# Kernel tuning notes

Hardware: AMD Instinct MI355X
Metric: run time of the kernel (lower is better)

Reference implementation:

```python
import jax, jax.numpy as jnp
import numpy as np

FEAT, HID, HEADS, OUT, NLAYERS = 32, 64, 6, 1, 4
NG, NP, K = 16, 1000, 10
EPS_BN, EPS_IN = 1e-5, 1e-5


def _build_graph(pos, rng=None):
    # knn_graph(k=10, loop=True, batch=batch) -> to_undirected -> add_self_loops
    N = NG * NP
    parts = []
    for g in range(NG):
        off = g * NP
        p = pos[off:off + NP]
        d2 = ((p[:, None, :] - p[None, :, :]) ** 2).sum(-1)
        nbr = np.argsort(d2, axis=1)[:, :K] + off  # includes self (loop=True)
        src = nbr.reshape(-1)
        dst = np.repeat(np.arange(NP) + off, K)
        parts.append(np.stack([src, dst]))
    ei = np.concatenate(parts, axis=1)
    und = np.unique(np.concatenate([ei, ei[::-1]], axis=1).T, axis=0).T  # to_undirected (coalesced)
    loops = np.tile(np.arange(N), (2, 1))  # add_self_loops (PyG appends unconditionally)
    return np.concatenate([und, loops], axis=1).astype(np.int64)


def setup_inputs() -> dict:
    rng = np.random.default_rng(0)
    N = NG * NP
    pos = rng.standard_normal((N, 3)).astype(np.float32)
    batch = np.repeat(np.arange(NG), NP).astype(np.int64)
    edge_index = _build_graph(pos)

    def lin(fi, fo):
        return (rng.standard_normal((fi, fo)) / np.sqrt(fi)).astype(np.float32)

    HC = HEADS * HID
    z = lambda *s: jnp.zeros(s, jnp.float32)
    o = lambda *s: jnp.ones(s, jnp.float32)
    return dict(
        x=jnp.asarray(rng.standard_normal((N, FEAT)).astype(np.float32)),
        pos=jnp.asarray(pos),
        w_lin1=jnp.asarray(lin(FEAT, HID)), b_lin1=z(HID),
        w_e1=jnp.asarray(lin(1, 32)), b_e1=z(32),
        w_e2=jnp.asarray(lin(32, 1)), b_e2=z(1),
        Wl=jnp.asarray(np.stack([lin(HID, HC) for _ in range(NLAYERS)])), bl=z(NLAYERS, HC),
        Wr=jnp.asarray(np.stack([lin(HID, HC) for _ in range(NLAYERS)])), br=z(NLAYERS, HC),
        We=jnp.asarray(np.stack([lin(1, HC) for _ in range(NLAYERS)])),
        att=jnp.asarray((rng.standard_normal((NLAYERS, HEADS, HID)) / np.sqrt(HID)).astype(np.float32)),
        b_gat=z(NLAYERS, HID),
        w_emb1=jnp.asarray(lin(HID, HID)), b_emb1=z(HID),
        bn1_g=o(HID), bn1_b=z(HID), bn1_m=z(HID), bn1_v=o(HID),
        w_emb2=jnp.asarray(lin(HID, HID)), b_emb2=z(HID),
        bn2_g=o(HID), bn2_b=z(HID), bn2_m=z(HID), bn2_v=o(HID),
        w_pred=jnp.asarray(lin(HID, OUT)), b_pred=z(OUT),
        edge_index=jnp.asarray(edge_index),
        batch=jnp.asarray(batch),
        n_graphs=NG,
    )


def _bn_eval(x, g, b, m, v):
    return (x - m) / jnp.sqrt(v + EPS_BN) * g + b


def _inorm(h, batch, n_graphs):
    # PyG InstanceNorm (affine=False): per-graph, per-channel standardization
    ones = jnp.ones((h.shape[0], 1), h.dtype)
    cnt = jax.ops.segment_sum(ones, batch, num_segments=n_graphs)
    mean = jax.ops.segment_sum(h, batch, num_segments=n_graphs) / cnt
    hc = h - mean[batch]
    var = jax.ops.segment_sum(hc * hc, batch, num_segments=n_graphs) / cnt
    return hc / jnp.sqrt(var[batch] + EPS_IN)


def _gatv2(h, src, dst, ea, Wl, bl, Wr, br, We, att, bias, n):
    # GATv2Conv(heads=HEADS, concat=False, edge_dim=1)
    xl = (h @ Wl + bl).reshape(-1, HEADS, HID)  # [N,H,C] source proj
    xr = (h @ Wr + br).reshape(-1, HEADS, HID)  # [N,H,C] target proj
    e = (ea @ We).reshape(-1, HEADS, HID)       # [E,H,C] edge proj (bias=False)
    g = jax.nn.leaky_relu(xl[src] + xr[dst] + e, 0.2)
    alpha = jnp.einsum('ehc,hc->eh', g, att)    # [E,H]
    amax = jax.ops.segment_max(alpha, dst, num_segments=n)
    ex = jnp.exp(alpha - amax[dst])
    den = jax.ops.segment_sum(ex, dst, num_segments=n)
    a = ex / (den[dst] + 1e-16)                 # PyG softmax eps
    out = jax.ops.segment_sum(xl[src] * a[:, :, None], dst, num_segments=n)
    return out.mean(axis=1) + bias              # concat=False -> head mean


def reference(x, pos, w_lin1, b_lin1, w_e1, b_e1, w_e2, b_e2, Wl, bl, Wr, br, We, att, b_gat,
              w_emb1, b_emb1, bn1_g, bn1_b, bn1_m, bn1_v, w_emb2, b_emb2,
              bn2_g, bn2_b, bn2_m, bn2_v, w_pred, b_pred, edge_index, batch, n_graphs):
    src, dst = edge_index[0], edge_index[1]
    d = pos[src] - pos[dst]
    s = (d * d).sum(-1, keepdims=True)
    ew = jnp.where(s == 0, 0.0, jnp.sqrt(jnp.where(s == 0, 1.0, s)))  # safe norm (0-grad at 0)
    m = jax.nn.relu(ew @ w_e1 + b_e1)            # MLP([1,32,1]) (BN in eval = identity)
    ea = jax.nn.relu(m @ w_e2 + b_e2)            # relu(edge_MLP(.)) -> [E,1]
    h = x @ w_lin1 + b_lin1
    n = h.shape[0]
    for i in range(NLAYERS):
        h = jax.nn.relu(h + _gatv2(h, src, dst, ea, Wl[i], bl[i], Wr[i], br[i], We[i], att[i], b_gat[i], n))
        h = _inorm(h, batch, n_graphs)
    z = jax.nn.relu(h @ w_emb1 + b_emb1)
    z = _bn_eval(z, bn1_g, bn1_b, bn1_m, bn1_v)
    h_out = z @ w_emb2 + b_emb2
    pred = _bn_eval(h_out, bn2_g, bn2_b, bn2_m, bn2_v) @ w_pred + b_pred
    return h_out, pred
```

## Files before the change

kernel.cpp:

```cpp
#include <hip/hip_runtime.h>
#include <hip/hip_bf16.h>
#include <stdint.h>

typedef __hip_bfloat16 bf16;
typedef __attribute__((ext_vector_type(8))) short short8;
typedef __attribute__((ext_vector_type(4))) float float4v;
__device__ __forceinline__ float bf(const bf16 x){ return __bfloat162float(x); }
__device__ __forceinline__ float bfu(uint32_t u){ u <<= 16; return __uint_as_float(u); }
__device__ __forceinline__ short f2bs(float v){
    bf16 b = __float2bfloat16(v);
    return *(short*)&b;
}

#define FEAT    32
#define HID     64
#define HEADS   6
#define HC      384
#define NLAYERS 4
#define NG      16
#define NP      1000
#define NN      16000
#define EPS_BN  1e-5f
#define EPS_IN  1e-5f
#define MNODE   16
#define LOG2E   1.44269504f
#define STATSZ  (2*NG*HID)
#define NBLK    (NN/4)

__device__ __forceinline__ float normv(float v, const float* st, int g, int c){
    if (!st) return v;
    float s  = st[g*HID + c];
    float s2 = st[NG*HID + g*HID + c];
    float mean = s*(1.f/NP);
    float var  = fmaxf(s2*(1.f/NP) - mean*mean, 0.f);
    return (v - mean)*rsqrtf(var + EPS_IN);
}

__global__ void sentinel_kernel(float* out, int n, float val){
    int i = blockIdx.x*256 + threadIdx.x;
    if (i < n) out[i] = val;
}

__global__ void zero_kernel(int* p, int n){
    int i = blockIdx.x*256 + threadIdx.x;
    if (i < n) p[i] = 0;
}

__global__ void detect_kernel(const int* ei, int* mode){
    __shared__ int nz;
    if (threadIdx.x == 0) nz = 0;
    __syncthreads();
    for (int i = 1 + 2*threadIdx.x; i < 1024; i += 512)
        if (ei[i] != 0) atomicAdd(&nz, 1);
    __syncthreads();
    if (threadIdx.x == 0) *mode = (nz == 0) ? 1 : 0;
}

__device__ __forceinline__ int load_idx(const int* ei, int idx, int mode){
    if (mode) return (int)((const long long*)ei)[idx];
    return ei[idx];
}

__global__ void count_kernel(const int* ei, const int* mode, int* deg, int E){
    int e = blockIdx.x*256 + threadIdx.x;
    if (e >= E) return;
    int d = load_idx(ei, E + e, *mode);
    if (d >= 0 && d < NN) atomicAdd(&deg[d], 1);
}

__global__ void scan_kernel(const int* deg, int* rowptr, int N){
    __shared__ int part[256];
    __shared__ int offs[256];
    int t = threadIdx.x;
    int chunk = (N + 255)/256;
    int lo = t*chunk, hi = lo + chunk; if (hi > N) hi = N;
    int s = 0;
    for (int i = lo; i < hi; i++) s += deg[i];
    part[t] = s;
    __syncthreads();
    if (t == 0){
        int r = 0;
        for (int i = 0; i < 256; i++){ offs[i] = r; r += part[i]; }
        rowptr[N] = r;
    }
    __syncthreads();
    int r = offs[t];
    for (int i = lo; i < hi; i++){ rowptr[i] = r; r += deg[i]; }
}

__global__ void scatter_ea_kernel(const int* ei, const float* pos,
                                  const float* w_e1, const float* b_e1,
                                  const float* w_e2, const float* b_e2,
                                  const int* rowptr, int* fill, const int* mode_p,
                                  int* csr_src, float* ea_csr, int E){
    int e = blockIdx.x*256 + threadIdx.x;
    if (e >= E) return;
    int mode = *mode_p;
    int s = load_idx(ei, e, mode);
    int d = load_idx(ei, E + e, mode);
    if (s < 0 || s >= NN || d < 0 || d >= NN) return;
    float dx = pos[s*3+0] - pos[d*3+0];
    float dy = pos[s*3+1] - pos[d*3+1];
    float dz = pos[s*3+2] - pos[d*3+2];
    float ss = dx*dx + dy*dy + dz*dz;
    float ew = (ss == 0.f) ? 0.f : sqrtf(ss);
    float acc = b_e2[0];
    #pragma unroll
    for (int j = 0; j < 32; j++){
        float m = ew*w_e1[j] + b_e1[j];
        m = m > 0.f ? m : 0.f;
        acc += m*w_e2[j];
    }
    acc = acc > 0.f ? acc : 0.f;
    int p = rowptr[d] + atomicAdd(&fill[d], 1);
    if (p < 0 || p >= E) return;
    csr_src[p] = s;
    ea_csr[p] = acc;
}

__global__ void lin1_kernel(const float* __restrict__ x,
                            const float* __restrict__ w1, const float* __restrict__ b1,
                            float* __restrict__ h, int N){
    int tid = blockIdx.x*256 + threadIdx.x;
    if (tid >= N*HID) return;
    int n = tid >> 6, c = tid & 63;
    float acc = b1[c];
    #pragma unroll
    for (int k = 0; k < FEAT; k++) acc += x[n*FEAT+k] * w1[k*HID+c];
    h[tid] = acc;
}

__global__ __launch_bounds__(256) void xlxr_mfma_kernel(
        const float* __restrict__ h, const float* __restrict__ statPrev,
        const float* __restrict__ Wl, const float* __restrict__ bl,
        const float* __restrict__ Wr, const float* __restrict__ br,
        bf16* __restrict__ xl, bf16* __restrict__ xr, int layer){
    int n0 = blockIdx.x*16;
    int wave = threadIdx.x >> 6;
    int lane = threadIdx.x & 63;
    int q = lane >> 4;
    int m = lane & 15;
    int node = n0 + m;
    int g = node / NP;

    short8 afrag[2];
    #pragma unroll
    for (int s = 0; s < 2; s++){
        const float* hp = h + (size_t)node*HID + s*32 + q*8;
        #pragma unroll
        for (int j = 0; j < 8; j++){
            float v = normv(hp[j], statPrev, g, s*32 + q*8 + j);
            afrag[s][j] = f2bs(v);
        }
    }

    const float* wlp = Wl + (size_t)layer*HID*HC;
    const float* wrp = Wr + (size_t)layer*HID*HC;
    const float* blp = bl + (size_t)layer*HC;
    const float* brp = br + (size_t)layer*HC;

    for (int t = wave*12; t < wave*12 + 12; t++){
        int col = t*16 + m;
        bool isR = col >= HC;
        int c2 = isR ? col - HC : col;
        const float* W = isR ? wrp : wlp;
        short8 bfrag[2];
        #pragma unroll
        for (int s = 0; s < 2; s++){
            #pragma unroll
            for (int j = 0; j < 8; j++)
                bfrag[s][j] = f2bs(W[(size_t)(s*32 + q*8 + j)*HC + c2]);
        }
        float4v acc = {0.f, 0.f, 0.f, 0.f};
        acc = __builtin_amdgcn_mfma_f32_16x16x32_bf16(afrag[0], bfrag[0], acc, 0, 0, 0);
        acc = __builtin_amdgcn_mfma_f32_16x16x32_bf16(afrag[1], bfrag[1], acc, 0, 0, 0);
        float bias = isR ? brp[c2] : blp[c2];
        bf16* dst = isR ? xr : xl;
        #pragma unroll
        for (int r = 0; r < 4; r++){
            int row = q*4 + r;
            dst[(size_t)(n0 + row)*HC + c2] = __float2bfloat16(acc[r] + bias);
        }
    }
}

__global__ __launch_bounds__(384) void xlxr_fb_kernel(
        const float* __restrict__ h, const float* __restrict__ statPrev,
        const float* __restrict__ Wl, const float* __restrict__ bl,
        bf16* __restrict__ xl, int layer){
    int n0 = blockIdx.x*MNODE;
    int o = threadIdx.x;
    __shared__ float hh[MNODE*HID];
    for (int i = o; i < MNODE*HID; i += 384){
        int m = i >> 6, k = i & 63;
        int node = n0 + m;
        hh[k*MNODE + m] = normv(h[(size_t)node*HID + k], statPrev, node/NP, k);
    }
    __syncthreads();
    const float* wl = Wl + (size_t)layer*HID*HC;
    float accl[MNODE];
    float bL = bl[layer*HC + o];
    #pragma unroll
    for (int m = 0; m < MNODE; m++) accl[m] = bL;
    for (int k = 0; k < HID; k++){
        float wlv = wl[k*HC + o];
        #pragma unroll
        for (int m = 0; m < MNODE; m++) accl[m] += hh[k*MNODE + m]*wlv;
    }
    #pragma unroll
    for (int m = 0; m < MNODE; m++)
        xl[(size_t)(n0+m)*HC + o] = __float2bfloat16(accl[m]);
}

__global__ __launch_bounds__(256) void agg_kernel(
        const bf16* __restrict__ xl, const bf16* __restrict__ xr,
        const int* __restrict__ rowptr,
        const int* __restrict__ csr_src,
        const float* __restrict__ ea_csr,
        const float* __restrict__ Wr, const float* __restrict__ br,
        const float* __restrict__ We, const float* __restrict__ att,
        const float* __restrict__ b_gat,
        float* __restrict__ h,
        const float* __restrict__ statPrev, float* __restrict__ partial,
        int layer){
    int wave = threadIdx.x >> 6, lane = threadIdx.x & 63;
    int n = blockIdx.x*4 + wave;
    int g = n / NP;
    int r0 = rowptr[n];
    int deg = rowptr[n+1] - r0;

    __shared__ float ps[4][2][HID];

    int hb = lane >> 5;
    int ob = hb*HID + ((lane & 31) << 1);

    float xrr[6], wer[6], atr[6];
    if (xr){
        const uint32_t* xr32 = (const uint32_t*)xr + (size_t)n*(HC/2);
        uint32_t u0 = xr32[lane], u1 = xr32[lane+64], u2 = xr32[lane+128];
        xrr[0] = bfu(u0 & 0xffffu); xrr[1] = bfu(u0 >> 16);
        xrr[2] = bfu(u1 & 0xffffu); xrr[3] = bfu(u1 >> 16);
        xrr[4] = bfu(u2 & 0xffffu); xrr[5] = bfu(u2 >> 16);
    } else {
        float hval = normv(h[(size_t)n*HID + lane], statPrev, g, lane);
        const float* wr = Wr + (size_t)layer*HID*HC;
        #pragma unroll
        for (int q = 0; q < 6; q++) xrr[q] = 0.f;
        for (int k = 0; k < HID; k++){
            float hk = __shfl(hval, k);
            #pragma unroll
            for (int q = 0; q < 3; q++){
                xrr[2*q]   += hk*wr[k*HC + ob + q*128];
                xrr[2*q+1] += hk*wr[k*HC + ob + q*128 + 1];
            }
        }
        #pragma unroll
        for (int q = 0; q < 3; q++){
            xrr[2*q]   += br[layer*HC + ob + q*128];
            xrr[2*q+1] += br[layer*HC + ob + q*128 + 1];
        }
    }
    #pragma unroll
    for (int q = 0; q < 3; q++){
        int o = layer*HC + ob + q*128;
        wer[2*q] = We[o];  wer[2*q+1] = We[o+1];
        atr[2*q] = att[o]*LOG2E; atr[2*q+1] = att[o+1]*LOG2E;
    }

    float m0 = -1e30f, m1 = -1e30f, m2 = -1e30f;
    float l0 = 0.f, l1 = 0.f, l2 = 0.f;
    float a0=0.f,a1=0.f,a2=0.f,a3=0.f,a4=0.f,a5=0.f;

    const uint32_t* xl32 = (const uint32_t*)xl;

    int j = 0;
    for (; j + 1 < deg; j += 2){
        int sa = csr_src[r0 + j], sb = csr_src[r0 + j + 1];
        float eva = ea_csr[r0 + j], evb = ea_csr[r0 + j + 1];
        const uint32_t* ra = xl32 + (size_t)sa*(HC/2);
        const uint32_t* rb = xl32 + (size_t)sb*(HC/2);
        uint32_t ua0 = ra[lane], ua1 = ra[lane+64], ua2 = ra[lane+128];
        uint32_t ub0 = rb[lane], ub1 = rb[lane+64], ub2 = rb[lane+128];
        float xa0 = bfu(ua0 & 0xffffu), xa1 = bfu(ua0 >> 16);
        float xa2 = bfu(ua1 & 0xffffu), xa3 = bfu(ua1 >> 16);
        float xa4 = bfu(ua2 & 0xffffu), xa5 = bfu(ua2 >> 16);
        float xb0 = bfu(ub0 & 0xffffu), xb1 = bfu(ub0 >> 16);
        float xb2 = bfu(ub1 & 0xffffu), xb3 = bfu(ub1 >> 16);
        float xb4 = bfu(ub2 & 0xffffu), xb5 = bfu(ub2 >> 16);
        float ga, ca0, ca1, ca2, cb0, cb1, cb2;
        ga = xa0 + xrr[0] + eva*wer[0]; ga = fmaxf(ga, 0.2f*ga); ca0  = ga*atr[0];
        ga = xa1 + xrr[1] + eva*wer[1]; ga = fmaxf(ga, 0.2f*ga); ca0 += ga*atr[1];
        ga = xa2 + xrr[2] + eva*wer[2]; ga = fmaxf(ga, 0.2f*ga); ca1  = ga*atr[2];
        ga = xa3 + xrr[3] + eva*wer[3]; ga = fmaxf(ga, 0.2f*ga); ca1 += ga*atr[3];
        ga = xa4 + xrr[4] + eva*wer[4]; ga = fmaxf(ga, 0.2f*ga); ca2  = ga*atr[4];
        ga = xa5 + xrr[5] + eva*wer[5]; ga = fmaxf(ga, 0.2f*ga); ca2 += ga*atr[5];
        ga = xb0 + xrr[0] + evb*wer[0]; ga = fmaxf(ga, 0.2f*ga); cb0  = ga*atr[0];
        ga = xb1 + xrr[1] + evb*wer[1]; ga = fmaxf(ga, 0.2f*ga); cb0 += ga*atr[1];
        ga = xb2 + xrr[2] + evb*wer[2]; ga = fmaxf(ga, 0.2f*ga); cb1  = ga*atr[2];
        ga = xb3 + xrr[3] + evb*wer[3]; ga = fmaxf(ga, 0.2f*ga); cb1 += ga*atr[3];
        ga = xb4 + xrr[4] + evb*wer[4]; ga = fmaxf(ga, 0.2f*ga); cb2  = ga*atr[4];
        ga = xb5 + xrr[5] + evb*wer[5]; ga = fmaxf(ga, 0.2f*ga); cb2 += ga*atr[5];
        #pragma unroll
        for (int mm = 1; mm <= 16; mm <<= 1){
            ca0 += __shfl_xor(ca0, mm); cb0 += __shfl_xor(cb0, mm);
            ca1 += __shfl_xor(ca1, mm); cb1 += __shfl_xor(cb1, mm);
            ca2 += __shfl_xor(ca2, mm); cb2 += __shfl_xor(cb2, mm);
        }
        float mn, r, pa, pb;
        mn = fmaxf(fmaxf(m0, ca0), cb0);
        r = exp2f(m0 - mn); pa = exp2f(ca0 - mn); pb = exp2f(cb0 - mn);
        l0 = l0*r + pa + pb;
        a0 = a0*r + pa*xa0 + pb*xb0; a1 = a1*r + pa*xa1 + pb*xb1; m0 = mn;
        mn = fmaxf(fmaxf(m1, ca1), cb1);
        r = exp2f(m1 - mn); pa = exp2f(ca1 - mn); pb = exp2f(cb1 - mn);
        l1 = l1*r + pa + pb;
        a2 = a2*r + pa*xa2 + pb*xb2; a3 = a3*r + pa*xa3 + pb*xb3; m1 = mn;
        mn = fmaxf(fmaxf(m2, ca2), cb2);
        r = exp2f(m2 - mn); pa = exp2f(ca2 - mn); pb = exp2f(cb2 - mn);
        l2 = l2*r + pa + pb;
        a4 = a4*r + pa*xa4 + pb*xb4; a5 = a5*r + pa*xa5 + pb*xb5; m2 = mn;
    }
    if (j < deg){
        int s = csr_src[r0 + j];
        float eav = ea_csr[r0 + j];
        const uint32_t* row = xl32 + (size_t)s*(HC/2);
        uint32_t u0 = row[lane], u1 = row[lane+64], u2 = row[lane+128];
        float x0 = bfu(u0 & 0xffffu), x1 = bfu(u0 >> 16);
        float x2 = bfu(u1 & 0xffffu), x3 = bfu(u1 >> 16);
        float x4 = bfu(u2 & 0xffffu), x5 = bfu(u2 >> 16);
        float g2v, c0, c1, c2;
        g2v = x0 + xrr[0] + eav*wer[0]; g2v = fmaxf(g2v, 0.2f*g2v); c0  = g2v*atr[0];
        g2v = x1 + xrr[1] + eav*wer[1]; g2v = fmaxf(g2v, 0.2f*g2v); c0 += g2v*atr[1];
        g2v = x2 + xrr[2] + eav*wer[2]; g2v = fmaxf(g2v, 0.2f*g2v); c1  = g2v*atr[2];
        g2v = x3 + xrr[3] + eav*wer[3]; g2v = fmaxf(g2v, 0.2f*g2v); c1 += g2v*atr[3];
        g2v = x4 + xrr[4] + eav*wer[4]; g2v = fmaxf(g2v, 0.2f*g2v); c2  = g2v*atr[4];
        g2v = x5 + xrr[5] + eav*wer[5]; g2v = fmaxf(g2v, 0.2f*g2v); c2 += g2v*atr[5];
        #pragma unroll
        for (int mm = 1; mm <= 16; mm <<= 1){
            c0 += __shfl_xor(c0, mm);
            c1 += __shfl_xor(c1, mm);
            c2 += __shfl_xor(c2, mm);
        }
        float mn, r, pp;
        mn = fmaxf(m0, c0); r = exp2f(m0 - mn); pp = exp2f(c0 - mn);
        l0 = l0*r + pp; a0 = a0*r + pp*x0; a1 = a1*r + pp*x1;
        mn = fmaxf(m1, c1); r = exp2f(m1 - mn); pp = exp2f(c1 - mn);
        l1 = l1*r + pp; a2 = a2*r + pp*x2; a3 = a3*r + pp*x3;
        mn = fmaxf(m2, c2); r = exp2f(m2 - mn); pp = exp2f(c2 - mn);
        l2 = l2*r + pp; a4 = a4*r + pp*x4; a5 = a5*r + pp*x5;
    }

    float v0 = a0/(l0+1e-16f) + a2/(l1+1e-16f) + a4/(l2+1e-16f);
    float v1 = a1/(l0+1e-16f) + a3/(l1+1e-16f) + a5/(l2+1e-16f);
    v0 += __shfl_xor(v0, 32);
    v1 += __shfl_xor(v1, 32);
    if (lane < 32){
        int c = lane << 1;
        float2 hv2 = *(const float2*)&h[(size_t)n*HID + c];
        float r0n = normv(hv2.x, statPrev, g, c);
        float r1n = normv(hv2.y, statPrev, g, c + 1);
        float o0 = r0n + v0*(1.f/HEADS) + b_gat[layer*HID + c];
        float o1 = r1n + v1*(1.f/HEADS) + b_gat[layer*HID + c + 1];
        o0 = o0 > 0.f ? o0 : 0.f;
        o1 = o1 > 0.f ? o1 : 0.f;
        *(float2*)&h[(size_t)n*HID + c] = make_float2(o0, o1);
        ps[wave][0][c] = o0;   ps[wave][0][c+1] = o1;
        ps[wave][1][c] = o0*o0; ps[wave][1][c+1] = o1*o1;
    }
    __syncthreads();
    if (threadIdx.x < HID){
        int c = threadIdx.x;
        float s  = ps[0][0][c] + ps[1][0][c] + ps[2][0][c] + ps[3][0][c];
        float s2 = ps[0][1][c] + ps[1][1][c] + ps[2][1][c] + ps[3][1][c];
        partial[(size_t)blockIdx.x*128 + c]      = s;
        partial[(size_t)blockIdx.x*128 + 64 + c] = s2;
    }
}

__global__ void stat_reduce_kernel(const float* __restrict__ partial,
                                   float* __restrict__ stat){
    int idx = blockIdx.x*256 + threadIdx.x;
    if (idx >= NG*HID) return;
    int g = idx >> 6, c = idx & 63;
    int b0 = g*(NP/4);
    float s = 0.f, s2 = 0.f;
    for (int b = 0; b < NP/4; b++){
        s  += partial[(size_t)(b0+b)*128 + c];
        s2 += partial[(size_t)(b0+b)*128 + 64 + c];
    }
    stat[g*HID + c] = s;
    stat[NG*HID + g*HID + c] = s2;
}

__global__ __launch_bounds__(256) void final_kernel(
        const float* __restrict__ h, const float* __restrict__ statPrev,
        const float* w1, const float* b1,
        const float* g1, const float* be1, const float* m1, const float* v1,
        const float* w2, const float* b2,
        const float* g2, const float* be2, const float* m2, const float* v2,
        const float* wp, const float* bp,
        float* out, int N){
    int wave = threadIdx.x >> 6, c = threadIdx.x & 63;
    int n = blockIdx.x*4 + wave;
    __shared__ float hr[4][HID], zr[4][HID];
    hr[wave][c] = normv(h[(size_t)n*HID + c], statPrev, n/NP, c);
    __syncthreads();
    float z = b1[c];
    #pragma unroll 8
    for (int k = 0; k < HID; k++) z += hr[wave][k]*w1[k*HID+c];
    z = z > 0.f ? z : 0.f;
    z = (z - m1[c]) / sqrtf(v1[c] + EPS_BN) * g1[c] + be1[c];
    zr[wave][c] = z;
    __syncthreads();
    float ho = b2[c];
    #pragma unroll 8
    for (int k = 0; k < HID; k++) ho += zr[wave][k]*w2[k*HID+c];
    out[(size_t)n*HID + c] = ho;
    float t = (ho - m2[c]) / sqrtf(v2[c] + EPS_BN) * g2[c] + be2[c];
    float p = t * wp[c];
    #pragma unroll
    for (int m = 32; m >= 1; m >>= 1) p += __shfl_xor(p, m);
    if (c == 0) out[(size_t)N*HID + n] = p + bp[0];
}

extern "C" void kernel_launch(void* const* d_in, const int* in_sizes, int n_in,
                              void* d_out, int out_size, void* d_ws, size_t ws_size,
                              hipStream_t stream){
    const float* x      = (const float*)d_in[0];
    const float* pos    = (const float*)d_in[1];
    const float* w_lin1 = (const float*)d_in[2];
    const float* b_lin1 = (const float*)d_in[3];
    const float* w_e1   = (const float*)d_in[4];
    const float* b_e1   = (const float*)d_in[5];
    const float* w_e2   = (const float*)d_in[6];
    const float* b_e2   = (const float*)d_in[7];
    const float* Wl     = (const float*)d_in[8];
    const float* bl     = (const float*)d_in[9];
    const float* Wr     = (const float*)d_in[10];
    const float* br     = (const float*)d_in[11];
    const float* We     = (const float*)d_in[12];
    const float* att    = (const float*)d_in[13];
    const float* b_gat  = (const float*)d_in[14];
    const float* w_emb1 = (const float*)d_in[15];
    const float* b_emb1 = (const float*)d_in[16];
    const float* bn1_g  = (const float*)d_in[17];
    const float* bn1_b  = (const float*)d_in[18];
    const float* bn1_m  = (const float*)d_in[19];
    const float* bn1_v  = (const float*)d_in[20];
    const float* w_emb2 = (const float*)d_in[21];
    const float* b_emb2 = (const float*)d_in[22];
    const float* bn2_g  = (const float*)d_in[23];
    const float* bn2_b  = (const float*)d_in[24];
    const float* bn2_m  = (const float*)d_in[25];
    const float* bn2_v  = (const float*)d_in[26];
    const float* w_pred = (const float*)d_in[27];
    const float* b_pred = (const float*)d_in[28];
    const int*   ei     = (const int*)d_in[29];

    const int N = in_sizes[0] / FEAT;
    const int E = in_sizes[29] / 2;
    int ob = (out_size + 255)/256;

    bool ok = (n_in >= 32) && (N == NN) && (E > N)
           && (in_sizes[1]  == 3*N)
           && (in_sizes[8]  == NLAYERS*HID*HC)
           && (in_sizes[13] == NLAYERS*HEADS*HID)
           && (in_sizes[27] == HID)
           && (out_size == N*HID + N);
    if (!ok){
        sentinel_kernel<<<ob, 256, 0, stream>>>((float*)d_out, out_size, 4000.0f);
        return;
    }

    char* p = (char*)d_ws;
    auto carve = [&](size_t bytes)->void*{
        void* r = (void*)p;
        p += (bytes + 255) & ~(size_t)255;
        return r;
    };
    int*   meta   = (int*)  carve((size_t)(2*N + 64)*4);
    float* stats  = (float*)carve((size_t)NLAYERS*STATSZ*4);
    float* partial= (float*)carve((size_t)NBLK*128*4);
    int*   rowptr = (int*)  carve((size_t)(N+1)*4);
    int*   csr_src= (int*)  carve((size_t)E*4);
    float* ea_csr = (float*)carve((size_t)E*4);
    float* h      = (float*)carve((size_t)N*HID*4);
    bf16*  xl     = (bf16*) carve((size_t)N*HC*2);
    size_t used_base = (size_t)(p - (char*)d_ws);
    bf16* xr = nullptr;
    if (used_base + (size_t)N*HC*2 + 256 <= ws_size)
        xr = (bf16*)carve((size_t)N*HC*2);

    if (used_base > ws_size){
        sentinel_kernel<<<ob, 256, 0, stream>>>((float*)d_out, out_size,
                                                5000.0f + (float)(ws_size >> 20));
        return;
    }

    int* mode = meta;
    int* deg  = meta + 64;
    int* fill = meta + 64 + N;

    zero_kernel<<<(2*N + 64 + 255)/256, 256, 0, stream>>>(meta, 2*N + 64);
    detect_kernel<<<1, 256, 0, stream>>>(ei, mode);

    int eb = (E + 255)/256;
    count_kernel<<<eb, 256, 0, stream>>>(ei, mode, deg, E);
    scan_kernel<<<1, 256, 0, stream>>>(deg, rowptr, N);
    scatter_ea_kernel<<<eb, 256, 0, stream>>>(ei, pos, w_e1, b_e1, w_e2, b_e2,
                                              rowptr, fill, mode, csr_src, ea_csr, E);

    int nb = (N*HID + 255)/256;
    lin1_kernel<<<nb, 256, 0, stream>>>(x, w_lin1, b_lin1, h, N);

    for (int l = 0; l < NLAYERS; l++){
        const float* statPrev = (l == 0) ? nullptr : stats + (size_t)(l-1)*STATSZ;
        float* statCur = stats + (size_t)l*STATSZ;
        if (xr)
            xlxr_mfma_kernel<<<N/16, 256, 0, stream>>>(h, statPrev, Wl, bl, Wr, br,
                                                       xl, xr, l);
        else
            xlxr_fb_kernel<<<N/MNODE, 384, 0, stream>>>(h, statPrev, Wl, bl, xl, l);
        agg_kernel<<<N/4, 256, 0, stream>>>(xl, xr, rowptr, csr_src, ea_csr,
                                            Wr, br, We, att, b_gat, h,
                                            statPrev, partial, l);
        stat_reduce_kernel<<<(NG*HID + 255)/256, 256, 0, stream>>>(partial, statCur);
    }

    final_kernel<<<N/4, 256, 0, stream>>>(h, stats + (size_t)(NLAYERS-1)*STATSZ,
        w_emb1, b_emb1, bn1_g, bn1_b, bn1_m, bn1_v,
        w_emb2, b_emb2, bn2_g, bn2_b, bn2_m, bn2_v,
        w_pred, b_pred, (float*)d_out, N);
}
```

Baseline: 556.3 us.

## Prepack GAT weights into MFMA fragments and remap aggregation lanes per head

Adds a one-time kernel that converts Wl/Wr to bf16 and stores them in MFMA B-fragment order, so the projection kernel loads two short8 vectors per tile instead of sixteen strided fp32 loads plus conversions. The h loads feeding the A fragment become float4. The aggregation kernel is remapped so each group of 8 lanes owns one head with 8 channels, loaded as uint4. This cuts the shuffle reduction to 3 steps and keeps one softmax state per lane. It leaves 16 of 64 lanes idle and adds a cross-group shuffle reduction of 8 values at the end.

```diff
diff --git a/kernel.cpp b/kernel.cpp
--- a/kernel.cpp
+++ b/kernel.cpp
@@ -26,6 +26,8 @@
 #define LOG2E   1.44269504f
 #define STATSZ  (2*NG*HID)
 #define NBLK    (NN/4)
+#define NTILES  48
+#define WPKSZ   (NLAYERS*NTILES*64*16)
 
 __device__ __forceinline__ float normv(float v, const float* st, int g, int c){
     if (!st) return v;
@@ -130,10 +132,34 @@
     h[tid] = acc;
 }
 
+__global__ void wpack_kernel(const float* __restrict__ Wl,
+                             const float* __restrict__ Wr,
+                             short* __restrict__ wpk){
+    int idx = blockIdx.x*256 + threadIdx.x;
+    if (idx >= NLAYERS*NTILES*64) return;
+    int layer = idx / (NTILES*64);
+    int r = idx - layer*NTILES*64;
+    int t = r >> 6, lane = r & 63;
+    int q = lane >> 4, m = lane & 15;
+    int col = t*16 + m;
+    bool isR = col >= HC;
+    int c2 = isR ? col - HC : col;
+    const float* W = (isR ? Wr : Wl) + (size_t)layer*HID*HC;
+    short out[16];
+    #pragma unroll
+    for (int s = 0; s < 2; s++)
+        #pragma unroll
+        for (int j = 0; j < 8; j++)
+            out[s*8+j] = f2bs(W[(size_t)(s*32 + q*8 + j)*HC + c2]);
+    short8* dst = (short8*)(wpk + (size_t)idx*16);
+    dst[0] = *(short8*)&out[0];
+    dst[1] = *(short8*)&out[8];
+}
+
 __global__ __launch_bounds__(256) void xlxr_mfma_kernel(
         const float* __restrict__ h, const float* __restrict__ statPrev,
-        const float* __restrict__ Wl, const float* __restrict__ bl,
-        const float* __restrict__ Wr, const float* __restrict__ br,
+        const short* __restrict__ wpk,
+        const float* __restrict__ bl, const float* __restrict__ br,
         bf16* __restrict__ xl, bf16* __restrict__ xr, int layer){
     int n0 = blockIdx.x*16;
     int wave = threadIdx.x >> 6;
@@ -146,34 +172,31 @@
     short8 afrag[2];
     #pragma unroll
     for (int s = 0; s < 2; s++){
-        const float* hp = h + (size_t)node*HID + s*32 + q*8;
-        #pragma unroll
-        for (int j = 0; j < 8; j++){
-            float v = normv(hp[j], statPrev, g, s*32 + q*8 + j);
-            afrag[s][j] = f2bs(v);
-        }
-    }
-
-    const float* wlp = Wl + (size_t)layer*HID*HC;
-    const float* wrp = Wr + (size_t)layer*HID*HC;
+        const float4* hp4 = (const float4*)(h + (size_t)node*HID + s*32 + q*8);
+        float4 va = hp4[0], vb = hp4[1];
+        int cb = s*32 + q*8;
+        afrag[s][0] = f2bs(normv(va.x, statPrev, g, cb+0));
+        afrag[s][1] = f2bs(normv(va.y, statPrev, g, cb+1));
+        afrag[s][2] = f2bs(normv(va.z, statPrev, g, cb+2));
+        afrag[s][3] = f2bs(normv(va.w, statPrev, g, cb+3));
+        afrag[s][4] = f2bs(normv(vb.x, statPrev, g, cb+4));
+        afrag[s][5] = f2bs(normv(vb.y, statPrev, g, cb+5));
+        afrag[s][6] = f2bs(normv(vb.z, statPrev, g, cb+6));
+        afrag[s][7] = f2bs(normv(vb.w, statPrev, g, cb+7));
+    }
+
     const float* blp = bl + (size_t)layer*HC;
     const float* brp = br + (size_t)layer*HC;
 
     for (int t = wave*12; t < wave*12 + 12; t++){
+        const short8* bsrc = (const short8*)(wpk + ((size_t)(layer*NTILES + t)*64 + lane)*16);
+        short8 b0 = bsrc[0], b1 = bsrc[1];
+        float4v acc = {0.f, 0.f, 0.f, 0.f};
+        acc = __builtin_amdgcn_mfma_f32_16x16x32_bf16(afrag[0], b0, acc, 0, 0, 0);
+        acc = __builtin_amdgcn_mfma_f32_16x16x32_bf16(afrag[1], b1, acc, 0, 0, 0);
         int col = t*16 + m;
         bool isR = col >= HC;
         int c2 = isR ? col - HC : col;
-        const float* W = isR ? wrp : wlp;
-        short8 bfrag[2];
-        #pragma unroll
-        for (int s = 0; s < 2; s++){
-            #pragma unroll
-            for (int j = 0; j < 8; j++)
-                bfrag[s][j] = f2bs(W[(size_t)(s*32 + q*8 + j)*HC + c2]);
-        }
-        float4v acc = {0.f, 0.f, 0.f, 0.f};
-        acc = __builtin_amdgcn_mfma_f32_16x16x32_bf16(afrag[0], bfrag[0], acc, 0, 0, 0);
-        acc = __builtin_amdgcn_mfma_f32_16x16x32_bf16(afrag[1], bfrag[1], acc, 0, 0, 0);
         float bias = isR ? brp[c2] : blp[c2];
         bf16* dst = isR ? xr : xl;
         #pragma unroll
@@ -231,141 +254,140 @@
 
     __shared__ float ps[4][2][HID];
 
-    int hb = lane >> 5;
-    int ob = hb*HID + ((lane & 31) << 1);
-
-    float xrr[6], wer[6], atr[6];
+    int grp = lane >> 3, li = lane & 7;
+    bool active = grp < HEADS;
+    int cb = active ? (grp*HID + li*8) : 0;
+
+    float xrr[8], wer[8], atr[8];
     if (xr){
-        const uint32_t* xr32 = (const uint32_t*)xr + (size_t)n*(HC/2);
-        uint32_t u0 = xr32[lane], u1 = xr32[lane+64], u2 = xr32[lane+128];
-        xrr[0] = bfu(u0 & 0xffffu); xrr[1] = bfu(u0 >> 16);
-        xrr[2] = bfu(u1 & 0xffffu); xrr[3] = bfu(u1 >> 16);
-        xrr[4] = bfu(u2 & 0xffffu); xrr[5] = bfu(u2 >> 16);
+        if (active){
+            const uint4* xru = (const uint4*)(xr + (size_t)n*HC);
+            uint4 u = xru[grp*8 + li];
+            xrr[0]=bfu(u.x&0xffffu); xrr[1]=bfu(u.x>>16);
+            xrr[2]=bfu(u.y&0xffffu); xrr[3]=bfu(u.y>>16);
+            xrr[4]=bfu(u.z&0xffffu); xrr[5]=bfu(u.z>>16);
+            xrr[6]=bfu(u.w&0xffffu); xrr[7]=bfu(u.w>>16);
+        }
     } else {
         float hval = normv(h[(size_t)n*HID + lane], statPrev, g, lane);
         const float* wr = Wr + (size_t)layer*HID*HC;
         #pragma unroll
-        for (int q = 0; q < 6; q++) xrr[q] = 0.f;
+        for (int i = 0; i < 8; i++) xrr[i] = 0.f;
         for (int k = 0; k < HID; k++){
             float hk = __shfl(hval, k);
             #pragma unroll
-            for (int q = 0; q < 3; q++){
-                xrr[2*q]   += hk*wr[k*HC + ob + q*128];
-                xrr[2*q+1] += hk*wr[k*HC + ob + q*128 + 1];
+            for (int i = 0; i < 8; i++) xrr[i] += hk*wr[k*HC + cb + i];
+        }
+        #pragma unroll
+        for (int i = 0; i < 8; i++) xrr[i] += br[layer*HC + cb + i];
+    }
+    #pragma unroll
+    for (int i = 0; i < 8; i++){
+        wer[i] = We[layer*HC + cb + i];
+        atr[i] = att[layer*HC + cb + i]*LOG2E;
+    }
+
+    float m_ = -1e30f, l_ = 0.f;
+    float acc[8];
+    #pragma unroll
+    for (int i = 0; i < 8; i++) acc[i] = 0.f;
+
+    const uint4* xlu = (const uint4*)xl;
+
+    if (active){
+        int j = 0;
+        for (; j + 1 < deg; j += 2){
+            int sa = csr_src[r0 + j], sb = csr_src[r0 + j + 1];
+            float eva = ea_csr[r0 + j], evb = ea_csr[r0 + j + 1];
+            uint4 ua = xlu[(size_t)sa*48 + grp*8 + li];
+            uint4 ub = xlu[(size_t)sb*48 + grp*8 + li];
+            float xa[8], xb[8];
+            xa[0]=bfu(ua.x&0xffffu); xa[1]=bfu(ua.x>>16);
+            xa[2]=bfu(ua.y&0xffffu); xa[3]=bfu(ua.y>>16);
+            xa[4]=bfu(ua.z&0xffffu); xa[5]=bfu(ua.z>>16);
+            xa[6]=bfu(ua.w&0xffffu); xa[7]=bfu(ua.w>>16);
+            xb[0]=bfu(ub.x&0xffffu); xb[1]=bfu(ub.x>>16);
+            xb[2]=bfu(ub.y&0xffffu); xb[3]=bfu(ub.y>>16);
+            xb[4]=bfu(ub.z&0xffffu); xb[5]=bfu(ub.z>>16);
+            xb[6]=bfu(ub.w&0xffffu); xb[7]=bfu(ub.w>>16);
+            float ca = 0.f, cb_ = 0.f;
+            #pragma unroll
+            for (int i = 0; i < 8; i++){
+                float ga = xa[i] + xrr[i] + eva*wer[i];
+                ga = fmaxf(ga, 0.2f*ga);
+                ca += ga*atr[i];
+                float gb = xb[i] + xrr[i] + evb*wer[i];
+                gb = fmaxf(gb, 0.2f*gb);
+                cb_ += gb*atr[i];
             }
+            #pragma unroll
+            for (int mm = 1; mm <= 4; mm <<= 1){
+                ca  += __shfl_xor(ca, mm);
+                cb_ += __shfl_xor(cb_, mm);
+            }
+            float mn = fmaxf(fmaxf(m_, ca), cb_);
+            float r  = exp2f(m_ - mn);
+            float pa = exp2f(ca - mn);
+            float pb = exp2f(cb_ - mn);
+            l_ = l_*r + pa + pb;
+            #pragma unroll
+            for (int i = 0; i < 8; i++) acc[i] = acc[i]*r + pa*xa[i] + pb*xb[i];
+            m_ = mn;
         }
-        #pragma unroll
-        for (int q = 0; q < 3; q++){
-            xrr[2*q]   += br[layer*HC + ob + q*128];
-            xrr[2*q+1] += br[layer*HC + ob + q*128 + 1];
+        if (j < deg){
+            int sa = csr_src[r0 + j];
+            float eva = ea_csr[r0 + j];
+            uint4 ua = xlu[(size_t)sa*48 + grp*8 + li];
+            float xa[8];
+            xa[0]=bfu(ua.x&0xffffu); xa[1]=bfu(ua.x>>16);
+            xa[2]=bfu(ua.y&0xffffu); xa[3]=bfu(ua.y>>16);
+            xa[4]=bfu(ua.z&0xffffu); xa[5]=bfu(ua.z>>16);
+            xa[6]=bfu(ua.w&0xffffu); xa[7]=bfu(ua.w>>16);
+            float ca = 0.f;
+            #pragma unroll
+            for (int i = 0; i < 8; i++){
+                float ga = xa[i] + xrr[i] + eva*wer[i];
+                ga = fmaxf(ga, 0.2f*ga);
+                ca += ga*atr[i];
+            }
+            #pragma unroll
+            for (int mm = 1; mm <= 4; mm <<= 1) ca += __shfl_xor(ca, mm);
+            float mn = fmaxf(m_, ca);
+            float r  = exp2f(m_ - mn);
+            float pa = exp2f(ca - mn);
+            l_ = l_*r + pa;
+            #pragma unroll
+            for (int i = 0; i < 8; i++) acc[i] = acc[i]*r + pa*xa[i];
+            m_ = mn;
         }
     }
-    #pragma unroll
-    for (int q = 0; q < 3; q++){
-        int o = layer*HC + ob + q*128;
-        wer[2*q] = We[o];  wer[2*q+1] = We[o+1];
-        atr[2*q] = att[o]*LOG2E; atr[2*q+1] = att[o+1]*LOG2E;
-    }
-
-    float m0 = -1e30f, m1 = -1e30f, m2 = -1e30f;
-    float l0 = 0.f, l1 = 0.f, l2 = 0.f;
-    float a0=0.f,a1=0.f,a2=0.f,a3=0.f,a4=0.f,a5=0.f;
-
-    const uint32_t* xl32 = (const uint32_t*)xl;
-
-    int j = 0;
-    for (; j + 1 < deg; j += 2){
-        int sa = csr_src[r0 + j], sb = csr_src[r0 + j + 1];
-        float eva = ea_csr[r0 + j], evb = ea_csr[r0 + j + 1];
-        const uint32_t* ra = xl32 + (size_t)sa*(HC/2);
-        const uint32_t* rb = xl32 + (size_t)sb*(HC/2);
-        uint32_t ua0 = ra[lane], ua1 = ra[lane+64], ua2 = ra[lane+128];
-        uint32_t ub0 = rb[lane], ub1 = rb[lane+64], ub2 = rb[lane+128];
-        float xa0 = bfu(ua0 & 0xffffu), xa1 = bfu(ua0 >> 16);
-        float xa2 = bfu(ua1 & 0xffffu), xa3 = bfu(ua1 >> 16);
-        float xa4 = bfu(ua2 & 0xffffu), xa5 = bfu(ua2 >> 16);
-        float xb0 = bfu(ub0 & 0xffffu), xb1 = bfu(ub0 >> 16);
-        float xb2 = bfu(ub1 & 0xffffu), xb3 = bfu(ub1 >> 16);
-        float xb4 = bfu(ub2 & 0xffffu), xb5 = bfu(ub2 >> 16);
-        float ga, ca0, ca1, ca2, cb0, cb1, cb2;
-        ga = xa0 + xrr[0] + eva*wer[0]; ga = fmaxf(ga, 0.2f*ga); ca0  = ga*atr[0];
-        ga = xa1 + xrr[1] + eva*wer[1]; ga = fmaxf(ga, 0.2f*ga); ca0 += ga*atr[1];
-        ga = xa2 + xrr[2] + eva*wer[2]; ga = fmaxf(ga, 0.2f*ga); ca1  = ga*atr[2];
-        ga = xa3 + xrr[3] + eva*wer[3]; ga = fmaxf(ga, 0.2f*ga); ca1 += ga*atr[3];
-        ga = xa4 + xrr[4] + eva*wer[4]; ga = fmaxf(ga, 0.2f*ga); ca2  = ga*atr[4];
-        ga = xa5 + xrr[5] + eva*wer[5]; ga = fmaxf(ga, 0.2f*ga); ca2 += ga*atr[5];
-        ga = xb0 + xrr[0] + evb*wer[0]; ga = fmaxf(ga, 0.2f*ga); cb0  = ga*atr[0];
-        ga = xb1 + xrr[1] + evb*wer[1]; ga = fmaxf(ga, 0.2f*ga); cb0 += ga*atr[1];
-        ga = xb2 + xrr[2] + evb*wer[2]; ga = fmaxf(ga, 0.2f*ga); cb1  = ga*atr[2];
-        ga = xb3 + xrr[3] + evb*wer[3]; ga = fmaxf(ga, 0.2f*ga); cb1 += ga*atr[3];
-        ga = xb4 + xrr[4] + evb*wer[4]; ga = fmaxf(ga, 0.2f*ga); cb2  = ga*atr[4];
-        ga = xb5 + xrr[5] + evb*wer[5]; ga = fmaxf(ga, 0.2f*ga); cb2 += ga*atr[5];
-        #pragma unroll
-        for (int mm = 1; mm <= 16; mm <<= 1){
-            ca0 += __shfl_xor(ca0, mm); cb0 += __shfl_xor(cb0, mm);
-            ca1 += __shfl_xor(ca1, mm); cb1 += __shfl_xor(cb1, mm);
-            ca2 += __shfl_xor(ca2, mm); cb2 += __shfl_xor(cb2, mm);
+
+    float v[8];
+    float rl = active ? 1.f/(l_ + 1e-16f) : 0.f;
+    #pragma unroll
+    for (int i = 0; i < 8; i++) v[i] = acc[i]*rl;
+    #pragma unroll
+    for (int mm = 8; mm <= 32; mm <<= 1)
+        #pragma unroll
+        for (int i = 0; i < 8; i++) v[i] += __shfl_xor(v[i], mm);
+
+    if (lane < 8){
+        int c0 = lane*8;
+        const float4* hp4 = (const float4*)(h + (size_t)n*HID + c0);
+        float4 h0 = hp4[0], h1 = hp4[1];
+        float hv[8] = {h0.x,h0.y,h0.z,h0.w,h1.x,h1.y,h1.z,h1.w};
+        float o[8];
+        #pragma unroll
+        for (int i = 0; i < 8; i++){
+            float r = normv(hv[i], statPrev, g, c0+i)
+                    + v[i]*(1.f/HEADS) + b_gat[layer*HID + c0 + i];
+            o[i] = r > 0.f ? r : 0.f;
+            ps[wave][0][c0+i] = o[i];
+            ps[wave][1][c0+i] = o[i]*o[i];
         }
-        float mn, r, pa, pb;
-        mn = fmaxf(fmaxf(m0, ca0), cb0);
-        r = exp2f(m0 - mn); pa = exp2f(ca0 - mn); pb = exp2f(cb0 - mn);
-        l0 = l0*r + pa + pb;
-        a0 = a0*r + pa*xa0 + pb*xb0; a1 = a1*r + pa*xa1 + pb*xb1; m0 = mn;
-        mn = fmaxf(fmaxf(m1, ca1), cb1);
-        r = exp2f(m1 - mn); pa = exp2f(ca1 - mn); pb = exp2f(cb1 - mn);
-        l1 = l1*r + pa + pb;
-        a2 = a2*r + pa*xa2 + pb*xb2; a3 = a3*r + pa*xa3 + pb*xb3; m1 = mn;
-        mn = fmaxf(fmaxf(m2, ca2), cb2);
-        r = exp2f(m2 - mn); pa = exp2f(ca2 - mn); pb = exp2f(cb2 - mn);
-        l2 = l2*r + pa + pb;
-        a4 = a4*r + pa*xa4 + pb*xb4; a5 = a5*r + pa*xa5 + pb*xb5; m2 = mn;
-    }
-    if (j < deg){
-        int s = csr_src[r0 + j];
-        float eav = ea_csr[r0 + j];
-        const uint32_t* row = xl32 + (size_t)s*(HC/2);
-        uint32_t u0 = row[lane], u1 = row[lane+64], u2 = row[lane+128];
-        float x0 = bfu(u0 & 0xffffu), x1 = bfu(u0 >> 16);
-        float x2 = bfu(u1 & 0xffffu), x3 = bfu(u1 >> 16);
-        float x4 = bfu(u2 & 0xffffu), x5 = bfu(u2 >> 16);
-        float g2v, c0, c1, c2;
-        g2v = x0 + xrr[0] + eav*wer[0]; g2v = fmaxf(g2v, 0.2f*g2v); c0  = g2v*atr[0];
-        g2v = x1 + xrr[1] + eav*wer[1]; g2v = fmaxf(g2v, 0.2f*g2v); c0 += g2v*atr[1];
-        g2v = x2 + xrr[2] + eav*wer[2]; g2v = fmaxf(g2v, 0.2f*g2v); c1  = g2v*atr[2];
-        g2v = x3 + xrr[3] + eav*wer[3]; g2v = fmaxf(g2v, 0.2f*g2v); c1 += g2v*atr[3];
-        g2v = x4 + xrr[4] + eav*wer[4]; g2v = fmaxf(g2v, 0.2f*g2v); c2  = g2v*atr[4];
-        g2v = x5 + xrr[5] + eav*wer[5]; g2v = fmaxf(g2v, 0.2f*g2v); c2 += g2v*atr[5];
-        #pragma unroll
-        for (int mm = 1; mm <= 16; mm <<= 1){
-            c0 += __shfl_xor(c0, mm);
-            c1 += __shfl_xor(c1, mm);
-            c2 += __shfl_xor(c2, mm);
-        }
-        float mn, r, pp;
-        mn = fmaxf(m0, c0); r = exp2f(m0 - mn); pp = exp2f(c0 - mn);
-        l0 = l0*r + pp; a0 = a0*r + pp*x0; a1 = a1*r + pp*x1;
-        mn = fmaxf(m1, c1); r = exp2f(m1 - mn); pp = exp2f(c1 - mn);
-        l1 = l1*r + pp; a2 = a2*r + pp*x2; a3 = a3*r + pp*x3;
-        mn = fmaxf(m2, c2); r = exp2f(m2 - mn); pp = exp2f(c2 - mn);
-        l2 = l2*r + pp; a4 = a4*r + pp*x4; a5 = a5*r + pp*x5;
-    }
-
-    float v0 = a0/(l0+1e-16f) + a2/(l1+1e-16f) + a4/(l2+1e-16f);
-    float v1 = a1/(l0+1e-16f) + a3/(l1+1e-16f) + a5/(l2+1e-16f);
-    v0 += __shfl_xor(v0, 32);
-    v1 += __shfl_xor(v1, 32);
-    if (lane < 32){
-        int c = lane << 1;
-        float2 hv2 = *(const float2*)&h[(size_t)n*HID + c];
-        float r0n = normv(hv2.x, statPrev, g, c);
-        float r1n = normv(hv2.y, statPrev, g, c + 1);
-        float o0 = r0n + v0*(1.f/HEADS) + b_gat[layer*HID + c];
-        float o1 = r1n + v1*(1.f/HEADS) + b_gat[layer*HID + c + 1];
-        o0 = o0 > 0.f ? o0 : 0.f;
-        o1 = o1 > 0.f ? o1 : 0.f;
-        *(float2*)&h[(size_t)n*HID + c] = make_float2(o0, o1);
-        ps[wave][0][c] = o0;   ps[wave][0][c+1] = o1;
-        ps[wave][1][c] = o0*o0; ps[wave][1][c+1] = o1*o1;
+        float4* out4 = (float4*)(h + (size_t)n*HID + c0);
+        out4[0] = make_float4(o[0],o[1],o[2],o[3]);
+        out4[1] = make_float4(o[4],o[5],o[6],o[7]);
     }
     __syncthreads();
     if (threadIdx.x < HID){
@@ -481,6 +503,7 @@
     int*   meta   = (int*)  carve((size_t)(2*N + 64)*4);
     float* stats  = (float*)carve((size_t)NLAYERS*STATSZ*4);
     float* partial= (float*)carve((size_t)NBLK*128*4);
+    short* wpk    = (short*)carve((size_t)WPKSZ*2);
     int*   rowptr = (int*)  carve((size_t)(N+1)*4);
     int*   csr_src= (int*)  carve((size_t)E*4);
     float* ea_csr = (float*)carve((size_t)E*4);
@@ -512,12 +535,13 @@
 
     int nb = (N*HID + 255)/256;
     lin1_kernel<<<nb, 256, 0, stream>>>(x, w_lin1, b_lin1, h, N);
+    wpack_kernel<<<(NLAYERS*NTILES*64 + 255)/256, 256, 0, stream>>>(Wl, Wr, wpk);
 
     for (int l = 0; l < NLAYERS; l++){
         const float* statPrev = (l == 0) ? nullptr : stats + (size_t)(l-1)*STATSZ;
         float* statCur = stats + (size_t)l*STATSZ;
         if (xr)
-            xlxr_mfma_kernel<<<N/16, 256, 0, stream>>>(h, statPrev, Wl, bl, Wr, br,
+            xlxr_mfma_kernel<<<N/16, 256, 0, stream>>>(h, statPrev, wpk, bl, br,
                                                        xl, xr, l);
         else
             xlxr_fb_kernel<<<N/MNODE, 384, 0, stream>>>(h, statPrev, Wl, bl, xl, l);
```

After: 518.2 us. -6.8%, faster.
